# Kernel optimization log

Hardware: AMD Instinct MI355X
Metric: run time of the kernel (lower is better)

Reference implementation:

```python
import jax, jax.numpy as jnp
import numpy as np

HEADS = 4
HID = 64
NEG_SLOPE = 0.2  # PyG GATConv default


def gat_layer(x, src, dst, W, att_src, att_dst, bias, heads, out_ch, concat):
    # x: [N, F_in]; src/dst: [E] (self-loops already appended)
    N = x.shape[0]
    xw = (x @ W).reshape(N, heads, out_ch)                     # [N, H, C]
    a_src = jnp.sum(xw * att_src, axis=-1)                     # [N, H]
    a_dst = jnp.sum(xw * att_dst, axis=-1)                     # [N, H]
    e = jax.nn.leaky_relu(a_src[src] + a_dst[dst], NEG_SLOPE)  # [E, H]
    # segment softmax over incoming edges of each destination node
    m = jax.ops.segment_max(e, dst, num_segments=N)            # [N, H]
    ex = jnp.exp(e - m[dst])
    s = jax.ops.segment_sum(ex, dst, num_segments=N)           # [N, H]
    alpha = ex / s[dst]                                        # [E, H]
    out = jax.ops.segment_sum(alpha[:, :, None] * xw[src], dst, num_segments=N)  # [N, H, C]
    if concat:
        out = out.reshape(N, heads * out_ch)
    else:
        out = out.mean(axis=1)
    return out + bias


def setup_inputs() -> dict:
    key = jax.random.key(0)
    ks = jax.random.split(key, 20)
    N, E, F_in, OUT = 50000, 800000, 128, 10
    H, C = HEADS, HID
    d = {}
    d['x'] = jax.random.normal(ks[0], (N, F_in), dtype=jnp.float32)
    d['edge_index'] = jax.random.randint(ks[1], (2, E), 0, N, dtype=jnp.int64)
    sc = 0.1
    d['W1'] = jax.random.normal(ks[2], (F_in, H * C), dtype=jnp.float32) * sc
    d['att_src1'] = jax.random.normal(ks[3], (H, C), dtype=jnp.float32) * sc
    d['att_dst1'] = jax.random.normal(ks[4], (H, C), dtype=jnp.float32) * sc
    d['b1'] = jnp.zeros((H * C,), dtype=jnp.float32)
    d['W2'] = jax.random.normal(ks[5], (H * C, H * C), dtype=jnp.float32) * sc
    d['att_src2'] = jax.random.normal(ks[6], (H, C), dtype=jnp.float32) * sc
    d['att_dst2'] = jax.random.normal(ks[7], (H, C), dtype=jnp.float32) * sc
    d['b2'] = jnp.zeros((H * C,), dtype=jnp.float32)
    d['W3'] = jax.random.normal(ks[8], (H * C, C), dtype=jnp.float32) * sc
    d['att_src3'] = jax.random.normal(ks[9], (1, C), dtype=jnp.float32) * sc
    d['att_dst3'] = jax.random.normal(ks[10], (1, C), dtype=jnp.float32) * sc
    d['b3'] = jnp.zeros((C,), dtype=jnp.float32)
    d['Wc'] = jax.random.normal(ks[11], (C, OUT), dtype=jnp.float32) * sc
    d['bc'] = jnp.zeros((OUT,), dtype=jnp.float32)
    return d


def reference(x, edge_index, W1, att_src1, att_dst1, b1, W2, att_src2, att_dst2, b2,
              W3, att_src3, att_dst3, b3, Wc, bc):
    N = x.shape[0]
    loop = jnp.arange(N, dtype=edge_index.dtype)
    src = jnp.concatenate([edge_index[0], loop])  # PyG default add_self_loops=True
    dst = jnp.concatenate([edge_index[1], loop])
    h = gat_layer(x, src, dst, W1, att_src1, att_dst1, b1, HEADS, HID, True)
    h = jax.nn.elu(h)  # dropout inactive (eval mode)
    h = gat_layer(h, src, dst, W2, att_src2, att_dst2, b2, HEADS, HID, True)
    h = jax.nn.elu(h)
    h = gat_layer(h, src, dst, W3, att_src3, att_dst3, b3, 1, HID, False)
    g = jnp.mean(h, axis=0, keepdims=True)  # [1, HID]
    return g @ Wc + bc
```

## Files before the change

### kernel.cpp

```cpp
#include <hip/hip_runtime.h>

#define NEG_SLOPE 0.2f

typedef __attribute__((ext_vector_type(8))) short bf16x8;
typedef __attribute__((ext_vector_type(4))) float f32x4;

__device__ __forceinline__ float bf2f(ushort u) {
  return __uint_as_float(((unsigned int)u) << 16);
}
__device__ __forceinline__ ushort f2bf(float f) {
  unsigned int u = __float_as_uint(f);
  u += 0x7fff + ((u >> 16) & 1);
  return (ushort)(u >> 16);
}
__device__ __forceinline__ float lrelu(float e) { return e > 0.f ? e : NEG_SLOPE * e; }

#if defined(__has_builtin)
#if __has_builtin(__builtin_amdgcn_cvt_f32_fp8) && __has_builtin(__builtin_amdgcn_cvt_pk_fp8_f32)
#define HW_FP8 1
#endif
#endif

__device__ __forceinline__ unsigned char ftofp8(float f) {
#ifdef HW_FP8
  unsigned int pk = __builtin_amdgcn_cvt_pk_fp8_f32(f, f, 0, false);
  return (unsigned char)(pk & 0xff);
#else
  float c = fminf(fmaxf(f, -448.f), 448.f);
  float y = c * 0x1.0p-120f;
  unsigned int u = __float_as_uint(y);
  unsigned int lsb = (u >> 20) & 1u;
  u += 0x7ffffu + lsb;
  return (unsigned char)(((u >> 24) & 0x80u) | ((u >> 20) & 0x7fu));
#endif
}

#ifdef HW_FP8
#define FP8DEC(u, s) __builtin_amdgcn_cvt_f32_fp8((u), (s))
#else
__device__ __forceinline__ float fp8dec_sw(unsigned int u, int sel) {
  unsigned int b = (u >> (8 * sel)) & 0xffu;
  unsigned int f = ((b & 0x80u) << 24) | ((b & 0x7fu) << 20);
  return __uint_as_float(f) * 0x1.0p+120f;
}
#define FP8DEC(u, s) fp8dec_sw((u), (s))
#endif

__device__ __forceinline__ float wave_max64(float v) {
  for (int off = 32; off; off >>= 1) v = fmaxf(v, __shfl_xor(v, off));
  return v;
}
__device__ __forceinline__ float wave_sum64(float v) {
  for (int off = 32; off; off >>= 1) v += __shfl_xor(v, off);
  return v;
}


__global__ void histoff_k(const int* __restrict__ ei, int E, int E2,
                          int* __restrict__ deg, int* __restrict__ eoff) {
  int i = blockIdx.x * 256 + threadIdx.x;
  if (i >= E2) return;
  int d = (i < E) ? ei[E + i] : (i - E);
  eoff[i] = atomicAdd(&deg[d], 1);
}

__global__ void scan1_k(const int* __restrict__ deg, int* __restrict__ excl,
                        int* __restrict__ bsum, int N) {
  __shared__ int sm[256];
  int t = threadIdx.x;
  int base = blockIdx.x * 1024 + t * 4;
  int v0 = (base + 0 < N) ? deg[base + 0] : 0;
  int v1 = (base + 1 < N) ? deg[base + 1] : 0;
  int v2 = (base + 2 < N) ? deg[base + 2] : 0;
  int v3 = (base + 3 < N) ? deg[base + 3] : 0;
  int tsum = v0 + v1 + v2 + v3;
  sm[t] = tsum;
  __syncthreads();
  for (int off = 1; off < 256; off <<= 1) {
    int x = (t >= off) ? sm[t - off] : 0;
    __syncthreads();
    sm[t] += x;
    __syncthreads();
  }
  int run = sm[t] - tsum;
  if (base + 0 < N) excl[base + 0] = run; run += v0;
  if (base + 1 < N) excl[base + 1] = run; run += v1;
  if (base + 2 < N) excl[base + 2] = run; run += v2;
  if (base + 3 < N) excl[base + 3] = run;
  if (t == 255) bsum[blockIdx.x] = sm[255];
}

__global__ void scan2_k(int* __restrict__ bsum, int nb) {
  int t = threadIdx.x;
  int orig = (t < nb) ? bsum[t] : 0;
  int v = orig;
  for (int off = 1; off < 64; off <<= 1) {
    int x = __shfl_up(v, off);
    if (t >= off) v += x;
  }
  if (t < nb) bsum[t] = v - orig;
}

__global__ void scan3_k(const int* __restrict__ excl, const int* __restrict__ bsum,
                        int* __restrict__ rowptr, int N, int E2) {
  int i = blockIdx.x * 256 + threadIdx.x;
  if (i < N) rowptr[i] = excl[i] + bsum[i >> 10];
  if (i == N) rowptr[N] = E2;
}

__global__ void scatter_k(const int* __restrict__ ei, int E, int E2,
                          const int* __restrict__ rowptr, const int* __restrict__ eoff,
                          int* __restrict__ csr_src) {
  int i = blockIdx.x * 256 + threadIdx.x;
  if (i >= E2) return;
  int s, d;
  if (i < E) { s = ei[i]; d = ei[E + i]; }
  else       { s = d = i - E; }
  csr_src[rowptr[d] + eoff[i]] = s;
}


__global__ void f2b_k(const float* __restrict__ in, ushort* __restrict__ out, int n4) {
  int i = blockIdx.x * 256 + threadIdx.x;
  if (i >= n4) return;
  float4 v = ((const float4*)in)[i];
  ushort4 o;
  o.x = f2bf(v.x); o.y = f2bf(v.y); o.z = f2bf(v.z); o.w = f2bf(v.w);
  ((ushort4*)out)[i] = o;
}

__global__ void wtrans3_k(const float* __restrict__ W1, const float* __restrict__ W2,
                          const float* __restrict__ W3, ushort* __restrict__ w1t,
                          ushort* __restrict__ w2t, ushort* __restrict__ w3t) {
  int z = blockIdx.z;
  const float* W = z == 0 ? W1 : z == 1 ? W2 : W3;
  ushort* Wt = z == 0 ? w1t : z == 1 ? w2t : w3t;
  int K = z == 0 ? 128 : 256;
  int Nc = z == 2 ? 64 : 256;
  int k = blockIdx.x * 16 + (threadIdx.x & 15);
  int n = blockIdx.y * 16 + (threadIdx.x >> 4);
  if (k < K && n < Nc) Wt[(size_t)n * K + k] = f2bf(W[(size_t)k * Nc + n]);
}


__global__ __launch_bounds__(256) void gemm_att(const ushort* __restrict__ A,
                                                const ushort* __restrict__ Bt,
                                                unsigned char* __restrict__ C,
                                                const float* __restrict__ att_s,
                                                const float* __restrict__ att_d,
                                                float* __restrict__ a_s,
                                                float* __restrict__ a_d,
                                                int M, int N, int K, int H) {
  __shared__ ushort As[128][72];
  __shared__ ushort Bs[64][72];
  int tid = threadIdx.x;
  int w = tid >> 6, l = tid & 63;
  int bm = blockIdx.y * 128, bn = blockIdx.x * 64;
  int fr = l & 15, fg = l >> 4, fk = fg * 8;
  f32x4 acc[2][4];
#pragma unroll
  for (int ar = 0; ar < 2; ++ar)
#pragma unroll
    for (int nb = 0; nb < 4; ++nb) acc[ar][nb] = (f32x4){0.f, 0.f, 0.f, 0.f};
  for (int k0 = 0; k0 < K; k0 += 64) {
#pragma unroll
    for (int i = 0; i < 4; ++i) {
      int s = tid + i * 256;
      int row = s >> 3, sc = (s & 7) * 8;
      bf16x8 v = {0, 0, 0, 0, 0, 0, 0, 0};
      if (bm + row < M) v = *(const bf16x8*)(A + (size_t)(bm + row) * K + k0 + sc);
      *(bf16x8*)&As[row][sc] = v;
    }
#pragma unroll
    for (int i = 0; i < 2; ++i) {
      int s = tid + i * 256;
      int row = s >> 3, sc = (s & 7) * 8;
      bf16x8 v = *(const bf16x8*)(Bt + (size_t)(bn + row) * K + k0 + sc);
      *(bf16x8*)&Bs[row][sc] = v;
    }
    __syncthreads();
#pragma unroll
    for (int kk = 0; kk < 64; kk += 32) {
      bf16x8 a0 = *(bf16x8*)&As[32 * w + fr][kk + fk];
      bf16x8 a1 = *(bf16x8*)&As[32 * w + 16 + fr][kk + fk];
#pragma unroll
      for (int nb = 0; nb < 4; ++nb) {
        bf16x8 b = *(bf16x8*)&Bs[nb * 16 + fr][kk + fk];
        acc[0][nb] = __builtin_amdgcn_mfma_f32_16x16x32_bf16(a0, b, acc[0][nb], 0, 0, 0);
        acc[1][nb] = __builtin_amdgcn_mfma_f32_16x16x32_bf16(a1, b, acc[1][nb], 0, 0, 0);
      }
    }
    __syncthreads();
  }
  int h = bn >> 6;
  float asc[4], adc[4];
#pragma unroll
  for (int nb = 0; nb < 4; ++nb) {
    asc[nb] = att_s[h * 64 + nb * 16 + fr];
    adc[nb] = att_d[h * 64 + nb * 16 + fr];
  }
#pragma unroll
  for (int ar = 0; ar < 2; ++ar) {
#pragma unroll
    for (int r = 0; r < 4; ++r) {
      float vs = 0.f, vd = 0.f;
#pragma unroll
      for (int nb = 0; nb < 4; ++nb) {
        vs = fmaf(acc[ar][nb][r], asc[nb], vs);
        vd = fmaf(acc[ar][nb][r], adc[nb], vd);
      }
#pragma unroll
      for (int off = 1; off < 16; off <<= 1) {
        vs += __shfl_xor(vs, off);
        vd += __shfl_xor(vd, off);
      }
      int row = bm + 32 * w + 16 * ar + fg * 4 + r;
      if (fr == 0 && row < M) {
        a_s[(size_t)row * H + h] = vs;
        a_d[(size_t)row * H + h] = vd;
      }
    }
#pragma unroll
    for (int nb = 0; nb < 4; ++nb)
#pragma unroll
      for (int r = 0; r < 4; ++r) {
        int row = bm + 32 * w + 16 * ar + fg * 4 + r;
        if (row < M) C[(size_t)row * N + bn + nb * 16 + fr] = ftofp8(acc[ar][nb][r]);
      }
  }
}


template <int WPB, int ACT>
__global__ __launch_bounds__(64 * WPB) void fagg4_k(
    const unsigned char* __restrict__ xw, const float4* __restrict__ a_s4,
    const float4* __restrict__ a_d4, const int* __restrict__ rowptr,
    const int* __restrict__ csr_src, const float* __restrict__ bias,
    ushort* __restrict__ hout, int N) {
  __shared__ float pbuf[WPB][4][66];
  int w = threadIdx.x >> 6, l = threadIdx.x & 63;
  int n = blockIdx.x * WPB + w;
  if (n >= N) return;
  int h = l >> 4;
  int beg = rowptr[n], end = rowptr[n + 1];
  int deg = end - beg;
  float4 ad = a_d4[n];
  f32x4 a0 = {0.f, 0.f, 0.f, 0.f}, a1 = {0.f, 0.f, 0.f, 0.f};
  f32x4 a2 = {0.f, 0.f, 0.f, 0.f}, a3 = {0.f, 0.f, 0.f, 0.f};
  const unsigned int* xwu = (const unsigned int*)xw;
  float s0, s1, s2, s3;

  if (deg <= 64) {
    int cnt = deg;
    float e0 = -1e30f, e1 = -1e30f, e2 = -1e30f, e3 = -1e30f;
    int sidx = 0;
    if (l < cnt) {
      sidx = csr_src[beg + l];
      float4 as = a_s4[sidx];
      e0 = lrelu(as.x + ad.x); e1 = lrelu(as.y + ad.y);
      e2 = lrelu(as.z + ad.z); e3 = lrelu(as.w + ad.w);
    }
    float m0 = wave_max64(e0), m1 = wave_max64(e1);
    float m2 = wave_max64(e2), m3 = wave_max64(e3);
    float p0 = __expf(e0 - m0), p1 = __expf(e1 - m1);
    float p2 = __expf(e2 - m2), p3 = __expf(e3 - m3);
    s0 = wave_sum64(p0); s1 = wave_sum64(p1);
    s2 = wave_sum64(p2); s3 = wave_sum64(p3);
    pbuf[w][0][l] = p0; pbuf[w][1][l] = p1;
    pbuf[w][2][l] = p2; pbuf[w][3][l] = p3;
    int j = 0;
    for (; j + 4 <= cnt; j += 4) {
      int t0 = __builtin_amdgcn_readlane(sidx, j);
      int t1 = __builtin_amdgcn_readlane(sidx, j + 1);
      int t2 = __builtin_amdgcn_readlane(sidx, j + 2);
      int t3 = __builtin_amdgcn_readlane(sidx, j + 3);
      float q0 = pbuf[w][h][j], q1 = pbuf[w][h][j + 1];
      float q2 = pbuf[w][h][j + 2], q3 = pbuf[w][h][j + 3];
      unsigned int u0 = xwu[(size_t)t0 * 64 + l];
      unsigned int u1 = xwu[(size_t)t1 * 64 + l];
      unsigned int u2 = xwu[(size_t)t2 * 64 + l];
      unsigned int u3 = xwu[(size_t)t3 * 64 + l];
      a0[0] = fmaf(q0, FP8DEC(u0, 0), a0[0]); a0[1] = fmaf(q0, FP8DEC(u0, 1), a0[1]);
      a0[2] = fmaf(q0, FP8DEC(u0, 2), a0[2]); a0[3] = fmaf(q0, FP8DEC(u0, 3), a0[3]);
      a1[0] = fmaf(q1, FP8DEC(u1, 0), a1[0]); a1[1] = fmaf(q1, FP8DEC(u1, 1), a1[1]);
      a1[2] = fmaf(q1, FP8DEC(u1, 2), a1[2]); a1[3] = fmaf(q1, FP8DEC(u1, 3), a1[3]);
      a2[0] = fmaf(q2, FP8DEC(u2, 0), a2[0]); a2[1] = fmaf(q2, FP8DEC(u2, 1), a2[1]);
      a2[2] = fmaf(q2, FP8DEC(u2, 2), a2[2]); a2[3] = fmaf(q2, FP8DEC(u2, 3), a2[3]);
      a3[0] = fmaf(q3, FP8DEC(u3, 0), a3[0]); a3[1] = fmaf(q3, FP8DEC(u3, 1), a3[1]);
      a3[2] = fmaf(q3, FP8DEC(u3, 2), a3[2]); a3[3] = fmaf(q3, FP8DEC(u3, 3), a3[3]);
    }
    for (; j < cnt; ++j) {
      int tj = __builtin_amdgcn_readlane(sidx, j);
      float qj = pbuf[w][h][j];
      unsigned int u = xwu[(size_t)tj * 64 + l];
      a0[0] = fmaf(qj, FP8DEC(u, 0), a0[0]); a0[1] = fmaf(qj, FP8DEC(u, 1), a0[1]);
      a0[2] = fmaf(qj, FP8DEC(u, 2), a0[2]); a0[3] = fmaf(qj, FP8DEC(u, 3), a0[3]);
    }
  } else {
    float m0 = -1e30f, m1 = -1e30f, m2 = -1e30f, m3 = -1e30f;
    for (int c0 = beg; c0 < end; c0 += 64) {
      int cnt = min(64, end - c0);
      float e0 = -1e30f, e1 = -1e30f, e2 = -1e30f, e3 = -1e30f;
      if (l < cnt) {
        float4 as = a_s4[csr_src[c0 + l]];
        e0 = lrelu(as.x + ad.x); e1 = lrelu(as.y + ad.y);
        e2 = lrelu(as.z + ad.z); e3 = lrelu(as.w + ad.w);
      }
      m0 = fmaxf(m0, wave_max64(e0)); m1 = fmaxf(m1, wave_max64(e1));
      m2 = fmaxf(m2, wave_max64(e2)); m3 = fmaxf(m3, wave_max64(e3));
    }
    s0 = s1 = s2 = s3 = 0.f;
    for (int c0 = beg; c0 < end; c0 += 64) {
      int cnt = min(64, end - c0);
      int sidx = 0;
      float p0 = 0.f, p1 = 0.f, p2 = 0.f, p3 = 0.f;
      if (l < cnt) {
        sidx = csr_src[c0 + l];
        float4 as = a_s4[sidx];
        p0 = __expf(lrelu(as.x + ad.x) - m0);
        p1 = __expf(lrelu(as.y + ad.y) - m1);
        p2 = __expf(lrelu(as.z + ad.z) - m2);
        p3 = __expf(lrelu(as.w + ad.w) - m3);
      }
      s0 += wave_sum64(p0); s1 += wave_sum64(p1);
      s2 += wave_sum64(p2); s3 += wave_sum64(p3);
      pbuf[w][0][l] = p0; pbuf[w][1][l] = p1;
      pbuf[w][2][l] = p2; pbuf[w][3][l] = p3;
      for (int j = 0; j < cnt; ++j) {
        int tj = __builtin_amdgcn_readlane(sidx, j);
        float qj = pbuf[w][h][j];
        unsigned int u = xwu[(size_t)tj * 64 + l];
        a0[0] = fmaf(qj, FP8DEC(u, 0), a0[0]); a0[1] = fmaf(qj, FP8DEC(u, 1), a0[1]);
        a0[2] = fmaf(qj, FP8DEC(u, 2), a0[2]); a0[3] = fmaf(qj, FP8DEC(u, 3), a0[3]);
      }
    }
  }

  float smy = h == 0 ? s0 : h == 1 ? s1 : h == 2 ? s2 : s3;
  float inv = 1.f / smy;
  float4 bv = ((const float4*)bias)[l];
  float o0 = ((a0[0] + a1[0]) + (a2[0] + a3[0])) * inv + bv.x;
  float o1 = ((a0[1] + a1[1]) + (a2[1] + a3[1])) * inv + bv.y;
  float o2 = ((a0[2] + a1[2]) + (a2[2] + a3[2])) * inv + bv.z;
  float o3 = ((a0[3] + a1[3]) + (a2[3] + a3[3])) * inv + bv.w;
  if (ACT) {
    o0 = o0 > 0.f ? o0 : __expf(o0) - 1.f;
    o1 = o1 > 0.f ? o1 : __expf(o1) - 1.f;
    o2 = o2 > 0.f ? o2 : __expf(o2) - 1.f;
    o3 = o3 > 0.f ? o3 : __expf(o3) - 1.f;
  }
  ushort4 ov;
  ov.x = f2bf(o0); ov.y = f2bf(o1); ov.z = f2bf(o2); ov.w = f2bf(o3);
  ((ushort4*)(hout + (size_t)n * 256))[l] = ov;
}


template <int WPB>
__global__ __launch_bounds__(64 * WPB) void fagg1_k(
    const unsigned char* __restrict__ xw, const float* __restrict__ a_s,
    const float* __restrict__ a_d, const int* __restrict__ rowptr,
    const int* __restrict__ csr_src, const float* __restrict__ bias,
    float* __restrict__ hout, int N) {
  __shared__ float pbuf[WPB][64];
  __shared__ int sbuf[WPB][64];
  int w = threadIdx.x >> 6, l = threadIdx.x & 63;
  int n = blockIdx.x * WPB + w;
  if (n >= N) return;
  int g = l >> 4, q = l & 15;
  int beg = rowptr[n], end = rowptr[n + 1];
  int deg = end - beg;
  float ad = a_d[n];
  f32x4 acc = {0.f, 0.f, 0.f, 0.f};
  const unsigned int* xwu = (const unsigned int*)xw;
  float ss;

  if (deg <= 64) {
    int cnt = deg;
    float e = -1e30f;
    int sidx = 0;
    if (l < cnt) {
      sidx = csr_src[beg + l];
      e = lrelu(a_s[sidx] + ad);
    }
    float m = wave_max64(e);
    float p = __expf(e - m);
    ss = wave_sum64(p);
    pbuf[w][l] = p;
    sbuf[w][l] = sidx;
    for (int j = 0; j < cnt; j += 4) {
      int jj = j + g;
      bool ok = jj < cnt;
      int idx = ok ? jj : 0;
      float pj = ok ? pbuf[w][idx] : 0.f;
      int sj = sbuf[w][idx];
      unsigned int u = xwu[(size_t)sj * 16 + q];
      acc[0] = fmaf(pj, FP8DEC(u, 0), acc[0]);
      acc[1] = fmaf(pj, FP8DEC(u, 1), acc[1]);
      acc[2] = fmaf(pj, FP8DEC(u, 2), acc[2]);
      acc[3] = fmaf(pj, FP8DEC(u, 3), acc[3]);
    }
  } else {
    float m = -1e30f;
    for (int c0 = beg; c0 < end; c0 += 64) {
      int cnt = min(64, end - c0);
      float e = -1e30f;
      if (l < cnt) e = lrelu(a_s[csr_src[c0 + l]] + ad);
      m = fmaxf(m, wave_max64(e));
    }
    ss = 0.f;
    for (int c0 = beg; c0 < end; c0 += 64) {
      int cnt = min(64, end - c0);
      int sidx = 0;
      float p = 0.f;
      if (l < cnt) {
        sidx = csr_src[c0 + l];
        p = __expf(lrelu(a_s[sidx] + ad) - m);
      }
      ss += wave_sum64(p);
      pbuf[w][l] = p;
      sbuf[w][l] = sidx;
      for (int j = 0; j < cnt; j += 4) {
        int jj = j + g;
        bool ok = jj < cnt;
        int idx = ok ? jj : 0;
        float pj = ok ? pbuf[w][idx] : 0.f;
        int sj = sbuf[w][idx];
        unsigned int u = xwu[(size_t)sj * 16 + q];
        acc[0] = fmaf(pj, FP8DEC(u, 0), acc[0]);
        acc[1] = fmaf(pj, FP8DEC(u, 1), acc[1]);
        acc[2] = fmaf(pj, FP8DEC(u, 2), acc[2]);
        acc[3] = fmaf(pj, FP8DEC(u, 3), acc[3]);
      }
    }
  }
#pragma unroll
  for (int i = 0; i < 4; ++i) {
    acc[i] += __shfl_xor(acc[i], 16);
    acc[i] += __shfl_xor(acc[i], 32);
  }
  float inv = 1.f / ss;
  float4 bv = ((const float4*)bias)[q];
  float4 o;
  o.x = acc[0] * inv + bv.x;
  o.y = acc[1] * inv + bv.y;
  o.z = acc[2] * inv + bv.z;
  o.w = acc[3] * inv + bv.w;
  if (g == 0) ((float4*)(hout + (size_t)n * 64))[q] = o;
}


__global__ void reduce_mean_k(const float* __restrict__ h3, float* __restrict__ g, int N) {
  __shared__ float sm[4][64];
  int w = threadIdx.x >> 6;
  int lane = threadIdx.x & 63;
  float acc = 0.f;
  for (int n = blockIdx.x * 4 + w; n < N; n += gridDim.x * 4)
    acc += h3[(size_t)n * 64 + lane];
  sm[w][lane] = acc;
  __syncthreads();
  if (w == 0) {
    float t = sm[0][lane] + sm[1][lane] + sm[2][lane] + sm[3][lane];
    atomicAdd(&g[lane], t);
  }
}

__global__ void final_k(const float* __restrict__ g, const float* __restrict__ Wc,
                        const float* __restrict__ bc, float* __restrict__ out, int N) {
  int lane = threadIdx.x;
  float gc = g[lane] / (float)N;
  for (int j = 0; j < 10; ++j) {
    float v = gc * Wc[lane * 10 + j];
    for (int off = 32; off; off >>= 1) v += __shfl_down(v, off);
    if (lane == 0) out[j] = v + bc[j];
  }
}


extern "C" void kernel_launch(void* const* d_in, const int* in_sizes, int n_in,
                              void* d_out, int out_size, void* d_ws, size_t ws_size,
                              hipStream_t stream) {
  const float* x   = (const float*)d_in[0];
  const int*   ei  = (const int*)d_in[1];
  const float* W1  = (const float*)d_in[2];
  const float* as1 = (const float*)d_in[3];
  const float* ad1 = (const float*)d_in[4];
  const float* b1  = (const float*)d_in[5];
  const float* W2  = (const float*)d_in[6];
  const float* as2 = (const float*)d_in[7];
  const float* ad2 = (const float*)d_in[8];
  const float* b2  = (const float*)d_in[9];
  const float* W3  = (const float*)d_in[10];
  const float* as3 = (const float*)d_in[11];
  const float* ad3 = (const float*)d_in[12];
  const float* b3  = (const float*)d_in[13];
  const float* Wc  = (const float*)d_in[14];
  const float* bc  = (const float*)d_in[15];
  float* out = (float*)d_out;

  int N = in_sizes[0] / 128;
  int E = in_sizes[1] / 2;
  int E2 = E + N;

  char* w = (char*)d_ws;
  auto alloc = [&](size_t bytes) {
    char* p = w;
    w += (bytes + 255) & ~(size_t)255;
    return p;
  };
  ushort* xb   = (ushort*)alloc((size_t)N * 128 * 2);
  float*  h3f  = (float*)xb;
  unsigned char* xw8 = (unsigned char*)alloc((size_t)N * 256);
  ushort* hb   = (ushort*)alloc((size_t)N * 256 * 2);
  ushort* w1t  = (ushort*)alloc((size_t)256 * 128 * 2);
  ushort* w2t  = (ushort*)alloc((size_t)256 * 256 * 2);
  ushort* w3t  = (ushort*)alloc((size_t)64 * 256 * 2);
  float*  a_s  = (float*)alloc((size_t)N * 4 * 4);
  float*  a_d  = (float*)alloc((size_t)N * 4 * 4);
  int*   deg    = (int*)alloc((size_t)N * 4);
  int*   excl   = (int*)alloc((size_t)N * 4);
  int*   bsum   = (int*)alloc(64 * 4);
  int*   rowptr = (int*)alloc((size_t)(N + 1) * 4);
  int*   eoff   = (int*)alloc((size_t)E2 * 4);
  int*   csr    = (int*)alloc((size_t)E2 * 4);
  float* g      = (float*)alloc(64 * 4);

  hipMemsetAsync(deg, 0, (size_t)N * 4, stream);
  hipMemsetAsync(g, 0, 64 * 4, stream);

  f2b_k<<<(N * 128 / 4 + 255) / 256, 256, 0, stream>>>(x, xb, N * 128 / 4);
  wtrans3_k<<<dim3(16, 16, 3), 256, 0, stream>>>(W1, W2, W3, w1t, w2t, w3t);

  int gE2 = (E2 + 255) / 256;
  histoff_k<<<gE2, 256, 0, stream>>>(ei, E, E2, deg, eoff);
  int nb = (N + 1023) / 1024;
  scan1_k<<<nb, 256, 0, stream>>>(deg, excl, bsum, N);
  scan2_k<<<1, 64, 0, stream>>>(bsum, nb);
  scan3_k<<<(N + 256) / 256, 256, 0, stream>>>(excl, bsum, rowptr, N, E2);
  scatter_k<<<gE2, 256, 0, stream>>>(ei, E, E2, rowptr, eoff, csr);

  int mb = (N + 127) / 128;
  int nwb = (N + 3) / 4;
  gemm_att<<<dim3(4, mb), 256, 0, stream>>>(xb, w1t, xw8, as1, ad1, a_s, a_d, N, 256, 128, 4);
  fagg4_k<4, 1><<<nwb, 256, 0, stream>>>(xw8, (const float4*)a_s, (const float4*)a_d,
                                         rowptr, csr, b1, hb, N);
  gemm_att<<<dim3(4, mb), 256, 0, stream>>>(hb, w2t, xw8, as2, ad2, a_s, a_d, N, 256, 256, 4);
  fagg4_k<4, 1><<<nwb, 256, 0, stream>>>(xw8, (const float4*)a_s, (const float4*)a_d,
                                         rowptr, csr, b2, hb, N);
  gemm_att<<<dim3(1, mb), 256, 0, stream>>>(hb, w3t, xw8, as3, ad3, a_s, a_d, N, 64, 256, 1);
  fagg1_k<4><<<nwb, 256, 0, stream>>>(xw8, a_s, a_d, rowptr, csr, b3, h3f, N);

  reduce_mean_k<<<256, 256, 0, stream>>>(h3f, g, N);
  final_k<<<1, 64, 0, stream>>>(g, Wc, bc, out, N);
}
```

Measured before the change: 369.4 us.

## Enlarge GEMM M-tile to 256 rows and use packed FP8 decode with packed FMA in aggregation

```diff
diff --git a/kernel.cpp b/kernel.cpp
--- a/kernel.cpp
+++ b/kernel.cpp
@@ -4,6 +4,7 @@
 
 typedef __attribute__((ext_vector_type(8))) short bf16x8;
 typedef __attribute__((ext_vector_type(4))) float f32x4;
+typedef __attribute__((ext_vector_type(2))) float f32x2;
 
 __device__ __forceinline__ float bf2f(ushort u) {
   return __uint_as_float(((unsigned int)u) << 16);
@@ -18,6 +19,9 @@
 #if defined(__has_builtin)
 #if __has_builtin(__builtin_amdgcn_cvt_f32_fp8) && __has_builtin(__builtin_amdgcn_cvt_pk_fp8_f32)
 #define HW_FP8 1
+#endif
+#if __has_builtin(__builtin_amdgcn_cvt_pk_f32_fp8)
+#define HW_PK8 1
 #endif
 #endif
 
@@ -45,6 +49,10 @@
 }
 #define FP8DEC(u, s) fp8dec_sw((u), (s))
 #endif
+
+__device__ __forceinline__ void pk_fma(f32x2& acc, f32x2 a, f32x2 b) {
+  asm("v_pk_fma_f32 %0, %1, %2, %0" : "+v"(acc) : "v"(a), "v"(b));
+}
 
 __device__ __forceinline__ float wave_max64(float v) {
   for (int off = 32; off; off >>= 1) v = fmaxf(v, __shfl_xor(v, off));
@@ -151,20 +159,20 @@
                                                 float* __restrict__ a_s,
                                                 float* __restrict__ a_d,
                                                 int M, int N, int K, int H) {
-  __shared__ ushort As[128][72];
+  __shared__ ushort As[256][72];
   __shared__ ushort Bs[64][72];
   int tid = threadIdx.x;
   int w = tid >> 6, l = tid & 63;
-  int bm = blockIdx.y * 128, bn = blockIdx.x * 64;
+  int bm = blockIdx.y * 256, bn = blockIdx.x * 64;
   int fr = l & 15, fg = l >> 4, fk = fg * 8;
-  f32x4 acc[2][4];
-#pragma unroll
-  for (int ar = 0; ar < 2; ++ar)
+  f32x4 acc[4][4];
+#pragma unroll
+  for (int ar = 0; ar < 4; ++ar)
 #pragma unroll
     for (int nb = 0; nb < 4; ++nb) acc[ar][nb] = (f32x4){0.f, 0.f, 0.f, 0.f};
   for (int k0 = 0; k0 < K; k0 += 64) {
 #pragma unroll
-    for (int i = 0; i < 4; ++i) {
+    for (int i = 0; i < 8; ++i) {
       int s = tid + i * 256;
       int row = s >> 3, sc = (s & 7) * 8;
       bf16x8 v = {0, 0, 0, 0, 0, 0, 0, 0};
@@ -181,14 +189,16 @@
     __syncthreads();
 #pragma unroll
     for (int kk = 0; kk < 64; kk += 32) {
-      bf16x8 a0 = *(bf16x8*)&As[32 * w + fr][kk + fk];
-      bf16x8 a1 = *(bf16x8*)&As[32 * w + 16 + fr][kk + fk];
-#pragma unroll
-      for (int nb = 0; nb < 4; ++nb) {
-        bf16x8 b = *(bf16x8*)&Bs[nb * 16 + fr][kk + fk];
-        acc[0][nb] = __builtin_amdgcn_mfma_f32_16x16x32_bf16(a0, b, acc[0][nb], 0, 0, 0);
-        acc[1][nb] = __builtin_amdgcn_mfma_f32_16x16x32_bf16(a1, b, acc[1][nb], 0, 0, 0);
-      }
+      bf16x8 af[4], bf[4];
+#pragma unroll
+      for (int ar = 0; ar < 4; ++ar) af[ar] = *(bf16x8*)&As[64 * w + 16 * ar + fr][kk + fk];
+#pragma unroll
+      for (int nb = 0; nb < 4; ++nb) bf[nb] = *(bf16x8*)&Bs[nb * 16 + fr][kk + fk];
+#pragma unroll
+      for (int ar = 0; ar < 4; ++ar)
+#pragma unroll
+        for (int nb = 0; nb < 4; ++nb)
+          acc[ar][nb] = __builtin_amdgcn_mfma_f32_16x16x32_bf16(af[ar], bf[nb], acc[ar][nb], 0, 0, 0);
     }
     __syncthreads();
   }
@@ -200,7 +210,7 @@
     adc[nb] = att_d[h * 64 + nb * 16 + fr];
   }
 #pragma unroll
-  for (int ar = 0; ar < 2; ++ar) {
+  for (int ar = 0; ar < 4; ++ar) {
 #pragma unroll
     for (int r = 0; r < 4; ++r) {
       float vs = 0.f, vd = 0.f;
@@ -214,7 +224,7 @@
         vs += __shfl_xor(vs, off);
         vd += __shfl_xor(vd, off);
       }
-      int row = bm + 32 * w + 16 * ar + fg * 4 + r;
+      int row = bm + 64 * w + 16 * ar + fg * 4 + r;
       if (fr == 0 && row < M) {
         a_s[(size_t)row * H + h] = vs;
         a_d[(size_t)row * H + h] = vd;
@@ -224,7 +234,7 @@
     for (int nb = 0; nb < 4; ++nb)
 #pragma unroll
       for (int r = 0; r < 4; ++r) {
-        int row = bm + 32 * w + 16 * ar + fg * 4 + r;
+        int row = bm + 64 * w + 16 * ar + fg * 4 + r;
         if (row < M) C[(size_t)row * N + bn + nb * 16 + fr] = ftofp8(acc[ar][nb][r]);
       }
   }
@@ -245,9 +255,9 @@
   int beg = rowptr[n], end = rowptr[n + 1];
   int deg = end - beg;
   float4 ad = a_d4[n];
-  f32x4 a0 = {0.f, 0.f, 0.f, 0.f}, a1 = {0.f, 0.f, 0.f, 0.f};
-  f32x4 a2 = {0.f, 0.f, 0.f, 0.f}, a3 = {0.f, 0.f, 0.f, 0.f};
   const unsigned int* xwu = (const unsigned int*)xw;
+  f32x2 aLo0 = {0.f, 0.f}, aHi0 = {0.f, 0.f}, aLo1 = {0.f, 0.f}, aHi1 = {0.f, 0.f};
+  f32x2 aLo2 = {0.f, 0.f}, aHi2 = {0.f, 0.f}, aLo3 = {0.f, 0.f}, aHi3 = {0.f, 0.f};
   float s0, s1, s2, s3;
 
   if (deg <= 64) {
@@ -269,6 +279,7 @@
     pbuf[w][0][l] = p0; pbuf[w][1][l] = p1;
     pbuf[w][2][l] = p2; pbuf[w][3][l] = p3;
     int j = 0;
+#ifdef HW_PK8
     for (; j + 4 <= cnt; j += 4) {
       int t0 = __builtin_amdgcn_readlane(sidx, j);
       int t1 = __builtin_amdgcn_readlane(sidx, j + 1);
@@ -280,22 +291,37 @@
       unsigned int u1 = xwu[(size_t)t1 * 64 + l];
       unsigned int u2 = xwu[(size_t)t2 * 64 + l];
       unsigned int u3 = xwu[(size_t)t3 * 64 + l];
-      a0[0] = fmaf(q0, FP8DEC(u0, 0), a0[0]); a0[1] = fmaf(q0, FP8DEC(u0, 1), a0[1]);
-      a0[2] = fmaf(q0, FP8DEC(u0, 2), a0[2]); a0[3] = fmaf(q0, FP8DEC(u0, 3), a0[3]);
-      a1[0] = fmaf(q1, FP8DEC(u1, 0), a1[0]); a1[1] = fmaf(q1, FP8DEC(u1, 1), a1[1]);
-      a1[2] = fmaf(q1, FP8DEC(u1, 2), a1[2]); a1[3] = fmaf(q1, FP8DEC(u1, 3), a1[3]);
-      a2[0] = fmaf(q2, FP8DEC(u2, 0), a2[0]); a2[1] = fmaf(q2, FP8DEC(u2, 1), a2[1]);
-      a2[2] = fmaf(q2, FP8DEC(u2, 2), a2[2]); a2[3] = fmaf(q2, FP8DEC(u2, 3), a2[3]);
-      a3[0] = fmaf(q3, FP8DEC(u3, 0), a3[0]); a3[1] = fmaf(q3, FP8DEC(u3, 1), a3[1]);
-      a3[2] = fmaf(q3, FP8DEC(u3, 2), a3[2]); a3[3] = fmaf(q3, FP8DEC(u3, 3), a3[3]);
+      f32x2 q; 
+      q = (f32x2){q0, q0};
+      pk_fma(aLo0, __builtin_amdgcn_cvt_pk_f32_fp8(u0, false), q);
+      pk_fma(aHi0, __builtin_amdgcn_cvt_pk_f32_fp8(u0, true), q);
+      q = (f32x2){q1, q1};
+      pk_fma(aLo1, __builtin_amdgcn_cvt_pk_f32_fp8(u1, false), q);
+      pk_fma(aHi1, __builtin_amdgcn_cvt_pk_f32_fp8(u1, true), q);
+      q = (f32x2){q2, q2};
+      pk_fma(aLo2, __builtin_amdgcn_cvt_pk_f32_fp8(u2, false), q);
+      pk_fma(aHi2, __builtin_amdgcn_cvt_pk_f32_fp8(u2, true), q);
+      q = (f32x2){q3, q3};
+      pk_fma(aLo3, __builtin_amdgcn_cvt_pk_f32_fp8(u3, false), q);
+      pk_fma(aHi3, __builtin_amdgcn_cvt_pk_f32_fp8(u3, true), q);
     }
     for (; j < cnt; ++j) {
       int tj = __builtin_amdgcn_readlane(sidx, j);
       float qj = pbuf[w][h][j];
       unsigned int u = xwu[(size_t)tj * 64 + l];
-      a0[0] = fmaf(qj, FP8DEC(u, 0), a0[0]); a0[1] = fmaf(qj, FP8DEC(u, 1), a0[1]);
-      a0[2] = fmaf(qj, FP8DEC(u, 2), a0[2]); a0[3] = fmaf(qj, FP8DEC(u, 3), a0[3]);
-    }
+      f32x2 q = {qj, qj};
+      pk_fma(aLo0, __builtin_amdgcn_cvt_pk_f32_fp8(u, false), q);
+      pk_fma(aHi0, __builtin_amdgcn_cvt_pk_f32_fp8(u, true), q);
+    }
+#else
+    for (; j < cnt; ++j) {
+      int tj = __builtin_amdgcn_readlane(sidx, j);
+      float qj = pbuf[w][h][j];
+      unsigned int u = xwu[(size_t)tj * 64 + l];
+      aLo0.x = fmaf(qj, FP8DEC(u, 0), aLo0.x); aLo0.y = fmaf(qj, FP8DEC(u, 1), aLo0.y);
+      aHi0.x = fmaf(qj, FP8DEC(u, 2), aHi0.x); aHi0.y = fmaf(qj, FP8DEC(u, 3), aHi0.y);
+    }
+#endif
   } else {
     float m0 = -1e30f, m1 = -1e30f, m2 = -1e30f, m3 = -1e30f;
     for (int c0 = beg; c0 < end; c0 += 64) {
@@ -330,19 +356,24 @@
         int tj = __builtin_amdgcn_readlane(sidx, j);
         float qj = pbuf[w][h][j];
         unsigned int u = xwu[(size_t)tj * 64 + l];
-        a0[0] = fmaf(qj, FP8DEC(u, 0), a0[0]); a0[1] = fmaf(qj, FP8DEC(u, 1), a0[1]);
-        a0[2] = fmaf(qj, FP8DEC(u, 2), a0[2]); a0[3] = fmaf(qj, FP8DEC(u, 3), a0[3]);
-      }
-    }
-  }
-
+        aLo0.x = fmaf(qj, FP8DEC(u, 0), aLo0.x); aLo0.y = fmaf(qj, FP8DEC(u, 1), aLo0.y);
+        aHi0.x = fmaf(qj, FP8DEC(u, 2), aHi0.x); aHi0.y = fmaf(qj, FP8DEC(u, 3), aHi0.y);
+      }
+    }
+  }
+
+  f32x2 aLo, aHi;
+  aLo.x = (aLo0.x + aLo1.x) + (aLo2.x + aLo3.x);
+  aLo.y = (aLo0.y + aLo1.y) + (aLo2.y + aLo3.y);
+  aHi.x = (aHi0.x + aHi1.x) + (aHi2.x + aHi3.x);
+  aHi.y = (aHi0.y + aHi1.y) + (aHi2.y + aHi3.y);
   float smy = h == 0 ? s0 : h == 1 ? s1 : h == 2 ? s2 : s3;
   float inv = 1.f / smy;
   float4 bv = ((const float4*)bias)[l];
-  float o0 = ((a0[0] + a1[0]) + (a2[0] + a3[0])) * inv + bv.x;
-  float o1 = ((a0[1] + a1[1]) + (a2[1] + a3[1])) * inv + bv.y;
-  float o2 = ((a0[2] + a1[2]) + (a2[2] + a3[2])) * inv + bv.z;
-  float o3 = ((a0[3] + a1[3]) + (a2[3] + a3[3])) * inv + bv.w;
+  float o0 = aLo.x * inv + bv.x;
+  float o1 = aLo.y * inv + bv.y;
+  float o2 = aHi.x * inv + bv.z;
+  float o3 = aHi.y * inv + bv.w;
   if (ACT) {
     o0 = o0 > 0.f ? o0 : __expf(o0) - 1.f;
     o1 = o1 > 0.f ? o1 : __expf(o1) - 1.f;
@@ -370,7 +401,7 @@
   int beg = rowptr[n], end = rowptr[n + 1];
   int deg = end - beg;
   float ad = a_d[n];
-  f32x4 acc = {0.f, 0.f, 0.f, 0.f};
+  f32x2 aLo = {0.f, 0.f}, aHi = {0.f, 0.f};
   const unsigned int* xwu = (const unsigned int*)xw;
   float ss;
 
@@ -394,10 +425,14 @@
       float pj = ok ? pbuf[w][idx] : 0.f;
       int sj = sbuf[w][idx];
       unsigned int u = xwu[(size_t)sj * 16 + q];
-      acc[0] = fmaf(pj, FP8DEC(u, 0), acc[0]);
-      acc[1] = fmaf(pj, FP8DEC(u, 1), acc[1]);
-      acc[2] = fmaf(pj, FP8DEC(u, 2), acc[2]);
-      acc[3] = fmaf(pj, FP8DEC(u, 3), acc[3]);
+#ifdef HW_PK8
+      f32x2 q2 = {pj, pj};
+      pk_fma(aLo, __builtin_amdgcn_cvt_pk_f32_fp8(u, false), q2);
+      pk_fma(aHi, __builtin_amdgcn_cvt_pk_f32_fp8(u, true), q2);
+#else
+      aLo.x = fmaf(pj, FP8DEC(u, 0), aLo.x); aLo.y = fmaf(pj, FP8DEC(u, 1), aLo.y);
+      aHi.x = fmaf(pj, FP8DEC(u, 2), aHi.x); aHi.y = fmaf(pj, FP8DEC(u, 3), aHi.y);
+#endif
     }
   } else {
     float m = -1e30f;
@@ -426,25 +461,26 @@
         float pj = ok ? pbuf[w][idx] : 0.f;
         int sj = sbuf[w][idx];
         unsigned int u = xwu[(size_t)sj * 16 + q];
-        acc[0] = fmaf(pj, FP8DEC(u, 0), acc[0]);
-        acc[1] = fmaf(pj, FP8DEC(u, 1), acc[1]);
-        acc[2] = fmaf(pj, FP8DEC(u, 2), acc[2]);
-        acc[3] = fmaf(pj, FP8DEC(u, 3), acc[3]);
-      }
-    }
-  }
-#pragma unroll
-  for (int i = 0; i < 4; ++i) {
-    acc[i] += __shfl_xor(acc[i], 16);
-    acc[i] += __shfl_xor(acc[i], 32);
+        aLo.x = fmaf(pj, FP8DEC(u, 0), aLo.x); aLo.y = fmaf(pj, FP8DEC(u, 1), aLo.y);
+        aHi.x = fmaf(pj, FP8DEC(u, 2), aHi.x); aHi.y = fmaf(pj, FP8DEC(u, 3), aHi.y);
+      }
+    }
+  }
+  float c0v = aLo.x, c1v = aLo.y, c2v = aHi.x, c3v = aHi.y;
+#pragma unroll
+  for (int off = 16; off <= 32; off <<= 1) {
+    c0v += __shfl_xor(c0v, off);
+    c1v += __shfl_xor(c1v, off);
+    c2v += __shfl_xor(c2v, off);
+    c3v += __shfl_xor(c3v, off);
   }
   float inv = 1.f / ss;
   float4 bv = ((const float4*)bias)[q];
   float4 o;
-  o.x = acc[0] * inv + bv.x;
-  o.y = acc[1] * inv + bv.y;
-  o.z = acc[2] * inv + bv.z;
-  o.w = acc[3] * inv + bv.w;
+  o.x = c0v * inv + bv.x;
+  o.y = c1v * inv + bv.y;
+  o.z = c2v * inv + bv.z;
+  o.w = c3v * inv + bv.w;
   if (g == 0) ((float4*)(hout + (size_t)n * 64))[q] = o;
 }
 
@@ -538,7 +574,7 @@
   scan3_k<<<(N + 256) / 256, 256, 0, stream>>>(excl, bsum, rowptr, N, E2);
   scatter_k<<<gE2, 256, 0, stream>>>(ei, E, E2, rowptr, eoff, csr);
 
-  int mb = (N + 127) / 128;
+  int mb = (N + 255) / 256;
   int nwb = (N + 3) / 4;
   gemm_att<<<dim3(4, mb), 256, 0, stream>>>(xb, w1t, xw8, as1, ad1, a_s, a_d, N, 256, 128, 4);
   fagg4_k<4, 1><<<nwb, 256, 0, stream>>>(xw8, (const float4*)a_s, (const float4*)a_d,
```

Result: slower. 389.4 us (+5.4%).
